# Kernel optimization log

Hardware: AMD Instinct MI355X
Metric: run time of the kernel (lower is better)

The kernel has to match this reference:

```python
import jax, jax.numpy as jnp
import numpy as np
import math

HEAD_DIM = 128
N_HEADS = 32
N_KV_HEADS = 8
HIDDEN = 4096
ROPE_BASE = 10000.0


def _rope_cos_sin(position_ids):
    # inv_freq: [D/2]
    inv_freq = 1.0 / (ROPE_BASE ** (jnp.arange(0, HEAD_DIM, 2, dtype=jnp.float32) / HEAD_DIM))
    freqs = position_ids.astype(jnp.float32)[..., None] * inv_freq  # [B,S,D/2]
    emb = jnp.concatenate([freqs, freqs], axis=-1)  # [B,S,D]
    return jnp.cos(emb), jnp.sin(emb)


def _rotate_half(x):
    x1, x2 = jnp.split(x, 2, axis=-1)
    return jnp.concatenate([-x2, x1], axis=-1)


def setup_inputs() -> dict:
    key = jax.random.key(0)
    ks = jax.random.split(key, 5)
    B, S = 1, 2048
    inp = {
        "hidden_states": jax.random.normal(ks[0], (B, S, HIDDEN), dtype=jnp.float32),
        "position_ids": jnp.arange(B * S, dtype=jnp.int32).reshape(B, S),
        "Wq": jax.random.normal(ks[1], (HIDDEN, N_HEADS * HEAD_DIM), dtype=jnp.float32) * 0.02,
        "Wk": jax.random.normal(ks[2], (HIDDEN, N_KV_HEADS * HEAD_DIM), dtype=jnp.float32) * 0.02,
        "Wv": jax.random.normal(ks[3], (HIDDEN, N_KV_HEADS * HEAD_DIM), dtype=jnp.float32) * 0.02,
        "Wo": jax.random.normal(ks[4], (N_HEADS * HEAD_DIM, HIDDEN), dtype=jnp.float32) * 0.02,
    }
    return inp


def reference(hidden_states, position_ids, Wq, Wk, Wv, Wo):
    B, S, _ = hidden_states.shape
    G = N_HEADS // N_KV_HEADS

    q = (hidden_states @ Wq).reshape(B, S, N_HEADS, HEAD_DIM).transpose(0, 2, 1, 3)      # [B,H,S,D]
    k = (hidden_states @ Wk).reshape(B, S, N_KV_HEADS, HEAD_DIM).transpose(0, 2, 1, 3)   # [B,Hkv,S,D]
    v = (hidden_states @ Wv).reshape(B, S, N_KV_HEADS, HEAD_DIM).transpose(0, 2, 1, 3)

    cos, sin = _rope_cos_sin(position_ids)          # [B,S,D]
    cos = cos[:, None, :, :]                         # [B,1,S,D]
    sin = sin[:, None, :, :]
    q = q * cos + _rotate_half(q) * sin
    k = k * cos + _rotate_half(k) * sin

    # GQA head expansion (repeat_interleave over head dim)
    k = jnp.repeat(k, G, axis=1)                     # [B,H,S,D]
    v = jnp.repeat(v, G, axis=1)

    scale = 1.0 / math.sqrt(HEAD_DIM)
    scores = jnp.einsum("bhqd,bhkd->bhqk", q, k) * scale  # [B,H,S,S]
    causal = jnp.triu(jnp.full((S, S), -jnp.inf, dtype=scores.dtype), k=1)
    scores = scores + causal[None, None]
    probs = jax.nn.softmax(scores.astype(jnp.float32), axis=-1).astype(q.dtype)
    ctx = jnp.einsum("bhqk,bhkd->bhqd", probs, v)    # [B,H,S,D]
    ctx = ctx.transpose(0, 2, 1, 3).reshape(B, S, N_HEADS * HEAD_DIM)
    return ctx @ Wo
```

## Files before the change

### kernel.cpp

```cpp
#include <hip/hip_runtime.h>
#include <hip/hip_bf16.h>
#include <math.h>

#define SEQ 2048
#define NHEADS 32
#define NKVH 8
#define HD 128
#define HIDDEN 4096

typedef unsigned short u16;
typedef unsigned int u32;
typedef __attribute__((ext_vector_type(8))) __bf16 bf16x8;
typedef __attribute__((ext_vector_type(4))) float f32x4;
typedef __attribute__((ext_vector_type(4))) u16 u16x4;
typedef __attribute__((ext_vector_type(4))) u32 u32x4;

__device__ __forceinline__ u16 f2bf(float f) {
  u32 u = __builtin_bit_cast(u32, f);
  u32 r = (u + 0x7fffu + ((u >> 16) & 1u)) >> 16;
  return (u16)r;
}
__device__ __forceinline__ float bf2f(u16 h) {
  return __builtin_bit_cast(float, ((u32)h) << 16);
}
__device__ __forceinline__ void gload_lds16(const void* g, void* l) {
  __builtin_amdgcn_global_load_lds(
      (const __attribute__((address_space(1))) u32*)g,
      (__attribute__((address_space(3))) u32*)l, 16, 0, 0);
}

__global__ void __launch_bounds__(256) conv_f2b_vec(const float* __restrict__ in,
                                                    u16* __restrict__ out, const int n) {
  const int i = (blockIdx.x * 256 + threadIdx.x) * 4;
  if (i >= n) return;
  const float4 v = *(const float4*)(in + i);
  u16x4 o;
  o.x = f2bf(v.x); o.y = f2bf(v.y); o.z = f2bf(v.z); o.w = f2bf(v.w);
  *(u16x4*)(out + i) = o;
}

__global__ void __launch_bounds__(256) trans_f2b(const float* __restrict__ in,
                                                 u16* __restrict__ out, const int R, const int C) {
  __shared__ float tile[32][33];
  const int c0 = blockIdx.x * 32, r0 = blockIdx.y * 32;
  const int tx = threadIdx.x & 31, ty = threadIdx.x >> 5;
#pragma unroll
  for (int i = 0; i < 4; ++i)
    tile[ty + i * 8][tx] = in[(size_t)(r0 + ty + i * 8) * C + c0 + tx];
  __syncthreads();
#pragma unroll
  for (int i = 0; i < 4; ++i)
    out[(size_t)(c0 + ty + i * 8) * R + r0 + tx] = f2bf(tile[tx][ty + i * 8]);
}

__global__ void __launch_bounds__(256) trans_b2b(const u16* __restrict__ in,
                                                 u16* __restrict__ out, const int R, const int C) {
  __shared__ u16 tile[32][34];
  const int c0 = blockIdx.x * 32, r0 = blockIdx.y * 32;
  const int tx = threadIdx.x & 31, ty = threadIdx.x >> 5;
#pragma unroll
  for (int i = 0; i < 4; ++i)
    tile[ty + i * 8][tx] = in[(size_t)(r0 + ty + i * 8) * C + c0 + tx];
  __syncthreads();
#pragma unroll
  for (int i = 0; i < 4; ++i)
    out[(size_t)(c0 + ty + i * 8) * R + r0 + tx] = tile[tx][ty + i * 8];
}

__global__ void __launch_bounds__(256) rope_ip(u16* __restrict__ x, const int* __restrict__ pos,
                                               const int lognh, const float oscale) {
  const int idx = blockIdx.x * 256 + threadIdx.x;
  const int j = idx & 63;
  const int hh = (idx >> 6) & ((1 << lognh) - 1);
  const int s = idx >> (6 + lognh);
  if (s >= SEQ) return;
  const float p = (float)pos[s];
  const float invf = __expf((float)j * -0.14391156831212787f);
  const float ang = p * invf;
  const float c = cosf(ang), sn = sinf(ang);
  u16* bp = x + ((size_t)s << (7 + lognh)) + hh * 128 + j;
  const float x1 = bf2f(bp[0]), x2 = bf2f(bp[64]);
  bp[0] = f2bf((x1 * c - x2 * sn) * oscale);
  bp[64] = f2bf((x2 * c + x1 * sn) * oscale);
}

template <int MF, int MH, int NH>
__device__ __forceinline__ void mfmaq(f32x4 (&acc)[MF][4], const bf16x8 (&af)[MF / 2][2],
                                      const bf16x8 (&bfv)[2][2]) {
#pragma unroll
  for (int f = 0; f < MF / 2; ++f)
#pragma unroll
    for (int e = 0; e < 2; ++e)
#pragma unroll
      for (int ks = 0; ks < 2; ++ks)
        acc[MH * (MF / 2) + f][NH * 2 + e] = __builtin_amdgcn_mfma_f32_16x16x32_bf16(
            af[f][ks], bfv[e][ks], acc[MH * (MF / 2) + f][NH * 2 + e], 0, 0, 0);
}

template <int MF>
__global__ void __launch_bounds__(512, 2) gemm8p(
    const u16* __restrict__ A, const u16* __restrict__ B0q, const u16* __restrict__ B1q,
    const u16* __restrict__ B2q, void* __restrict__ C0, void* __restrict__ C1,
    void* __restrict__ C2, const int K, const int n0t, const int n1t,
    const int N0, const int N1, const int N2, const int write_f32) {
  constexpr int BM = MF * 32;
  constexpr int AHR = BM / 2;
  constexpr int GA = (AHR * 128) / 8192;
  __shared__ u16 As[2][2][AHR * 64];
  __shared__ u16 Bs[2][2][128 * 64];

  const int t = threadIdx.x;
  const int lane = t & 63;
  const int w = t >> 6;
  const int wr = w >> 2;
  const int wc = w & 3;
  const int l15 = lane & 15, l4 = lane >> 4;

  const int nxt = gridDim.x;
  int flat = blockIdx.y * nxt + blockIdx.x;
  flat = (flat & 7) * ((nxt * (int)gridDim.y) >> 3) + (flat >> 3);
  int bxt = flat % nxt;
  const int byt = flat / nxt;

  const u16* Bp; char* Cw; int Nn;
  if (bxt < n0t) { Bp = B0q; Cw = (char*)C0; Nn = N0; }
  else if (bxt < n0t + n1t) { bxt -= n0t; Bp = B1q; Cw = (char*)C1; Nn = N1; }
  else { bxt -= n0t + n1t; Bp = B2q; Cw = (char*)C2; Nn = N2; }
  const int row0 = byt * BM, col0 = bxt * 256;

  auto stageA = [&](int buf, int half, int tile) {
#pragma unroll
    for (int g = 0; g < GA; ++g) {
      const int o = (g * 512 + t) * 16;
      const int ridx = o >> 7;
      const int slot = (o >> 4) & 7;
      const int gr = (ridx / (MF * 8)) * AHR + half * (MF * 8) + (ridx % (MF * 8));
      gload_lds16(A + (size_t)(row0 + gr) * K + (tile << 6) + ((slot ^ (ridx & 7)) << 3),
                  (char*)&As[buf][half][0] + o);
    }
  };
  auto stageB = [&](int buf, int half, int tile) {
#pragma unroll
    for (int g = 0; g < 2; ++g) {
      const int o = (g * 512 + t) * 16;
      const int ridx = o >> 7;
      const int slot = (o >> 4) & 7;
      const int gn = (ridx >> 5) * 64 + half * 32 + (ridx & 31);
      gload_lds16(Bp + (size_t)(col0 + gn) * K + (tile << 6) + ((slot ^ (ridx & 7)) << 3),
                  (char*)&Bs[buf][half][0] + o);
    }
  };

  bf16x8 af[MF / 2][2], bfv[2][2];
  auto loadA = [&](int buf, int half) {
#pragma unroll
    for (int f = 0; f < MF / 2; ++f)
#pragma unroll
      for (int ks = 0; ks < 2; ++ks) {
        const int idx = wr * (MF * 8) + f * 16 + l15;
        af[f][ks] = *(const bf16x8*)((const char*)&As[buf][half][0] + idx * 128 +
                                     (((ks * 4 + l4) ^ (idx & 7)) << 4));
      }
  };
  auto loadB = [&](int buf, int half) {
#pragma unroll
    for (int e = 0; e < 2; ++e)
#pragma unroll
      for (int ks = 0; ks < 2; ++ks) {
        const int idx = wc * 32 + e * 16 + l15;
        bfv[e][ks] = *(const bf16x8*)((const char*)&Bs[buf][half][0] + idx * 128 +
                                      (((ks * 4 + l4) ^ (idx & 7)) << 4));
      }
  };

  f32x4 acc[MF][4];
#pragma unroll
  for (int m_ = 0; m_ < MF; ++m_)
#pragma unroll
    for (int n_ = 0; n_ < 4; ++n_) acc[m_][n_] = f32x4{0.f, 0.f, 0.f, 0.f};

  const int nkt = K >> 6, nit = nkt >> 1;

#define VMW_STEADY                                                  \
  if constexpr (MF == 8) asm volatile("s_waitcnt vmcnt(4)" ::: "memory"); \
  else asm volatile("s_waitcnt vmcnt(3)" ::: "memory");
#define BAR __builtin_amdgcn_s_barrier()
#define PRIO1 __builtin_amdgcn_s_setprio(1)
#define PRIO0 __builtin_amdgcn_s_setprio(0)

  stageA(0, 0, 0); stageA(0, 1, 0); stageB(0, 0, 0); stageB(0, 1, 0);
  stageA(1, 0, 1); stageB(1, 1, 1);
  VMW_STEADY;
  BAR;

  for (int i = 0; i < nit; ++i) {
    const int tb = 2 * i;
    const bool g2 = (i + 1 < nit);
    loadA(0, 0); loadB(0, 0);
    stageA(1, 1, tb + 1);
    BAR; PRIO1; mfmaq<MF, 0, 0>(acc, af, bfv); PRIO0; BAR;
    loadB(0, 1);
    stageB(1, 0, tb + 1);
    BAR; PRIO1; mfmaq<MF, 0, 1>(acc, af, bfv); PRIO0; BAR;
    loadA(0, 1);
    if (g2) stageA(0, 0, tb + 2);
    BAR; PRIO1; mfmaq<MF, 1, 1>(acc, af, bfv); PRIO0; BAR;
    loadB(0, 0);
    if (g2) stageB(0, 1, tb + 2);
    BAR; PRIO1; mfmaq<MF, 1, 0>(acc, af, bfv); PRIO0;
    if (g2) { VMW_STEADY; } else { asm volatile("s_waitcnt vmcnt(0)" ::: "memory"); }
    BAR;
    loadA(1, 0); loadB(1, 0);
    if (g2) stageA(0, 1, tb + 2);
    BAR; PRIO1; mfmaq<MF, 0, 0>(acc, af, bfv); PRIO0; BAR;
    loadB(1, 1);
    if (g2) stageB(0, 0, tb + 2);
    BAR; PRIO1; mfmaq<MF, 0, 1>(acc, af, bfv); PRIO0; BAR;
    loadA(1, 1);
    if (g2) stageA(1, 0, tb + 3);
    BAR; PRIO1; mfmaq<MF, 1, 1>(acc, af, bfv); PRIO0; BAR;
    loadB(1, 0);
    if (g2) stageB(1, 1, tb + 3);
    BAR; PRIO1; mfmaq<MF, 1, 0>(acc, af, bfv); PRIO0;
    if (g2) { VMW_STEADY; } else { asm volatile("s_waitcnt vmcnt(0)" ::: "memory"); }
    BAR;
  }
#undef VMW_STEADY
#undef BAR
#undef PRIO1
#undef PRIO0

  if (write_f32) {
    float* C = (float*)Cw;
#pragma unroll
    for (int am = 0; am < MF; ++am) {
      const int row = row0 + wr * AHR + (am / (MF / 2)) * (MF * 8) + (am % (MF / 2)) * 16 + l4 * 4;
#pragma unroll
      for (int an = 0; an < 4; ++an) {
        const int col = col0 + wc * 64 + (an >> 1) * 32 + (an & 1) * 16 + l15;
#pragma unroll
        for (int r = 0; r < 4; ++r)
          C[(size_t)(row + r) * Nn + col] = acc[am][an][r];
      }
    }
  } else {
    u16* C = (u16*)Cw;
#pragma unroll
    for (int am = 0; am < MF; ++am) {
      const int row = row0 + wr * AHR + (am / (MF / 2)) * (MF * 8) + (am % (MF / 2)) * 16 + l4 * 4;
#pragma unroll
      for (int an = 0; an < 4; ++an) {
        const int col = col0 + wc * 64 + (an >> 1) * 32 + (an & 1) * 16 + l15;
#pragma unroll
        for (int r = 0; r < 4; ++r)
          C[(size_t)(row + r) * Nn + col] = f2bf(acc[am][an][r]);
      }
    }
  }
}

__device__ __forceinline__ void stage_kv(const u16* __restrict__ k, const u16* __restrict__ vt,
                                         const int kvh, const int kv0, u16* KsB, u16* VsB,
                                         const int t) {
#pragma unroll
  for (int i = 0; i < 4; ++i) {
    const int o = (i * 256 + t) * 16;
    const int row = o >> 8;
    const int slot = (o >> 4) & 15;
    gload_lds16(k + (size_t)(kv0 + row) * (NKVH * HD) + kvh * HD + ((slot ^ (row & 7)) << 3),
                (char*)KsB + o);
  }
#pragma unroll
  for (int i = 0; i < 4; ++i) {
    const int o = (i * 256 + t) * 16;
    const int row = o >> 7;
    const int slot = (o >> 4) & 7;
    gload_lds16(vt + (size_t)(kvh * HD + row) * SEQ + kv0 + ((slot ^ (row & 7)) << 3),
                (char*)VsB + o);
  }
}

__global__ void __launch_bounds__(256) attn_fwd(const u16* __restrict__ q, const u16* __restrict__ k,
                                                const u16* __restrict__ vt, u16* __restrict__ ctx) {
  __shared__ u16 Ks[2][64 * 128];
  __shared__ u16 Vs[2][128 * 64];
  const int t = threadIdx.x, lane = t & 63, w = t >> 6;
  const int h = blockIdx.x;
  const int qb = (int)gridDim.y - 1 - (int)blockIdx.y;
  const int kvh = h >> 2;
  const int q0 = qb * 64;
  const int sq_base = q0 + w * 16;
  const int l15 = lane & 15, l4 = lane >> 4;
  const int sq_abs = sq_base + l15;

  bf16x8 qf[4];
  {
    const u16* qp = q + (size_t)sq_abs * (NHEADS * HD) + h * HD + l4 * 8;
#pragma unroll
    for (int kb = 0; kb < 4; ++kb) qf[kb] = *(const bf16x8*)(qp + kb * 32);
  }
  f32x4 po[8];
#pragma unroll
  for (int i = 0; i < 8; ++i) po[i] = f32x4{0.f, 0.f, 0.f, 0.f};
  float mrow = -1e30f;
  float lrow = 0.f;

  const int nb = qb + 1;
  stage_kv(k, vt, kvh, 0, Ks[0], Vs[0], t);
  __syncthreads();
  int cur = 0;

  for (int b = 0; b < nb; ++b) {
    if (b + 1 < nb) stage_kv(k, vt, kvh, (b + 1) * 64, Ks[cur ^ 1], Vs[cur ^ 1], t);

    f32x4 st[4];
#pragma unroll
    for (int c = 0; c < 4; ++c) st[c] = f32x4{0.f, 0.f, 0.f, 0.f};
#pragma unroll
    for (int c = 0; c < 4; ++c) {
      const int row = c * 16 + l15;
#pragma unroll
      for (int kb = 0; kb < 4; ++kb) {
        const int slot = kb * 4 + l4;
        bf16x8 bk = *(const bf16x8*)((const char*)Ks[cur] + row * 256 + ((slot ^ (row & 7)) << 4));
        st[c] = __builtin_amdgcn_mfma_f32_16x16x32_bf16(bk, qf[kb], st[c], 0, 0, 0);
      }
    }

    if (b == nb - 1) {
#pragma unroll
      for (int c = 0; c < 4; ++c)
#pragma unroll
        for (int r = 0; r < 4; ++r) {
          const int sk = b * 64 + c * 16 + l4 * 4 + r;
          if (sk > sq_abs) st[c][r] = -1e30f;
        }
    }

    float rmax = -3e38f;
#pragma unroll
    for (int c = 0; c < 4; ++c)
      rmax = fmaxf(rmax, fmaxf(fmaxf(st[c][0], st[c][1]), fmaxf(st[c][2], st[c][3])));
    rmax = fmaxf(rmax, __shfl_xor(rmax, 16, 64));
    rmax = fmaxf(rmax, __shfl_xor(rmax, 32, 64));

    const bool skip = __all(rmax <= mrow + 8.f);
    const float mnew = skip ? mrow : fmaxf(mrow, rmax);

    float rs = 0.f;
#pragma unroll
    for (int c = 0; c < 4; ++c) {
      const float e0 = exp2f(st[c][0] - mnew), e1 = exp2f(st[c][1] - mnew);
      const float e2 = exp2f(st[c][2] - mnew), e3 = exp2f(st[c][3] - mnew);
      st[c][0] = e0; st[c][1] = e1; st[c][2] = e2; st[c][3] = e3;
      rs += (e0 + e1) + (e2 + e3);
    }
    rs += __shfl_xor(rs, 16, 64);
    rs += __shfl_xor(rs, 32, 64);

    if (!skip) {
      const float alpha = exp2f(mrow - mnew);
      mrow = mnew;
      lrow = lrow * alpha + rs;
      float av[4];
#pragma unroll
      for (int r = 0; r < 4; ++r) av[r] = __shfl(alpha, l4 * 4 + r, 16);
#pragma unroll
      for (int db = 0; db < 8; ++db)
#pragma unroll
        for (int r = 0; r < 4; ++r) po[db][r] *= av[r];
    } else {
      lrow += rs;
    }

    u32 pk[4][2];
#pragma unroll
    for (int c = 0; c < 4; ++c) {
      pk[c][0] = (u32)f2bf(st[c][0]) | ((u32)f2bf(st[c][1]) << 16);
      pk[c][1] = (u32)f2bf(st[c][2]) | ((u32)f2bf(st[c][3]) << 16);
    }
    const int src01 = l15 + ((lane & 16) << 1);
    const int src23 = src01 + 16;
    const bool lo = (lane & 32) == 0;
#pragma unroll
    for (int kb2 = 0; kb2 < 2; ++kb2) {
      const int c0 = kb2 * 2, c1 = c0 + 1;
      const u32 a0 = (u32)__shfl((int)pk[c0][0], src01, 64);
      const u32 a1 = (u32)__shfl((int)pk[c0][1], src01, 64);
      const u32 a2 = (u32)__shfl((int)pk[c0][0], src23, 64);
      const u32 a3 = (u32)__shfl((int)pk[c0][1], src23, 64);
      const u32 b0 = (u32)__shfl((int)pk[c1][0], src01, 64);
      const u32 b1 = (u32)__shfl((int)pk[c1][1], src01, 64);
      const u32 b2 = (u32)__shfl((int)pk[c1][0], src23, 64);
      const u32 b3 = (u32)__shfl((int)pk[c1][1], src23, 64);
      u32x4 wq;
      wq.x = lo ? a0 : b0;
      wq.y = lo ? a1 : b1;
      wq.z = lo ? a2 : b2;
      wq.w = lo ? a3 : b3;
      const bf16x8 pa = __builtin_bit_cast(bf16x8, wq);
#pragma unroll
      for (int db = 0; db < 8; ++db) {
        const int vrow = db * 16 + l15;
        const int pslot = kb2 * 4 + l4;
        bf16x8 bv = *(const bf16x8*)((const char*)Vs[cur] + vrow * 128 + ((pslot ^ (vrow & 7)) << 4));
        po[db] = __builtin_amdgcn_mfma_f32_16x16x32_bf16(pa, bv, po[db], 0, 0, 0);
      }
    }
    __syncthreads();
    cur ^= 1;
  }

  float rl[4];
#pragma unroll
  for (int r = 0; r < 4; ++r) rl[r] = 1.f / __shfl(lrow, l4 * 4 + r, 16);
#pragma unroll
  for (int db = 0; db < 8; ++db)
#pragma unroll
    for (int r = 0; r < 4; ++r) {
      const int sq = sq_base + l4 * 4 + r;
      const int d = db * 16 + l15;
      ctx[(size_t)sq * (NHEADS * HD) + h * HD + d] = f2bf(po[db][r] * rl[r]);
    }
}

extern "C" void kernel_launch(void* const* d_in, const int* in_sizes, int n_in,
                              void* d_out, int out_size, void* d_ws, size_t ws_size,
                              hipStream_t stream) {
  const float* hs = (const float*)d_in[0];
  const int* pos = (const int*)d_in[1];
  const float* Wq = (const float*)d_in[2];
  const float* Wk = (const float*)d_in[3];
  const float* Wv = (const float*)d_in[4];
  const float* Wo = (const float*)d_in[5];

  u16* ws = (u16*)d_ws;
  u16* Xb = ws;
  u16* Wqt = Xb + (size_t)2048 * 4096;
  u16* Wkt = Wqt + (size_t)4096 * 4096;
  u16* Wvt = Wkt + (size_t)1024 * 4096;
  u16* Wot = Wvt + (size_t)1024 * 4096;
  u16* qb = Wot + (size_t)4096 * 4096;
  u16* kb = qb + (size_t)2048 * 4096;
  u16* vb = kb + (size_t)2048 * 1024;
  u16* vtb = vb + (size_t)2048 * 1024;
  u16* ctx = vtb + (size_t)1024 * 2048;
  const size_t need = ((size_t)(ctx - ws) + (size_t)2048 * 4096) * 2;
  if (ws_size < need) return;

  conv_f2b_vec<<<8192, 256, 0, stream>>>(hs, Xb, 2048 * 4096);
  trans_f2b<<<dim3(128, 128), 256, 0, stream>>>(Wq, Wqt, 4096, 4096);
  trans_f2b<<<dim3(32, 128), 256, 0, stream>>>(Wk, Wkt, 4096, 1024);
  trans_f2b<<<dim3(32, 128), 256, 0, stream>>>(Wv, Wvt, 4096, 1024);
  trans_f2b<<<dim3(128, 128), 256, 0, stream>>>(Wo, Wot, 4096, 4096);

  gemm8p<8><<<dim3(24, 8), 512, 0, stream>>>(Xb, Wqt, Wkt, Wvt, qb, kb, vb,
                                             4096, 16, 4, 4096, 1024, 1024, 0);

  const float qscale = 0.08838834764831845f * 1.44269504088896340f;
  rope_ip<<<16384, 256, 0, stream>>>(qb, pos, 5, qscale);
  rope_ip<<<4096, 256, 0, stream>>>(kb, pos, 3, 1.0f);

  trans_b2b<<<dim3(32, 64), 256, 0, stream>>>(vb, vtb, 2048, 1024);

  attn_fwd<<<dim3(32, 32), 256, 0, stream>>>(qb, kb, vtb, ctx);

  gemm8p<4><<<dim3(16, 16), 512, 0, stream>>>(ctx, Wot, Wot, Wot, d_out, d_out, d_out,
                                              4096, 16, 0, 4096, 4096, 4096, 1);
}
```

Baseline: 375.7 us.

## Switch QKV GEMM to 32x32 MFMA and overlap Wo transpose in spare blocks

Rewrites the fused QKV projection GEMM to use 32x32x16 bf16 MFMA instructions with per-wave 128x64 tiles instead of 16x16x32. This reduces LDS fragment reads per flop and the MFMA issue count. The grid is padded from 192 to 256 blocks, and the 64 extra blocks do the Wo fp32-to-bf16 transpose, which removes a separate launch and fills otherwise idle CUs. The output GEMM becomes a specialized non-templated kernel. The transpose blocks run a serial 64-step loop and could become the tail of the QKV launch.

```diff
diff --git a/kernel.cpp b/kernel.cpp
--- a/kernel.cpp
+++ b/kernel.cpp
@@ -12,6 +12,7 @@
 typedef unsigned int u32;
 typedef __attribute__((ext_vector_type(8))) __bf16 bf16x8;
 typedef __attribute__((ext_vector_type(4))) float f32x4;
+typedef __attribute__((ext_vector_type(16))) float f32x16;
 typedef __attribute__((ext_vector_type(4))) u16 u16x4;
 typedef __attribute__((ext_vector_type(4))) u32 u32x4;
 
@@ -28,6 +29,11 @@
       (const __attribute__((address_space(1))) u32*)g,
       (__attribute__((address_space(3))) u32*)l, 16, 0, 0);
 }
+
+#define BAR __builtin_amdgcn_s_barrier()
+#define PRIO1 __builtin_amdgcn_s_setprio(1)
+#define PRIO0 __builtin_amdgcn_s_setprio(0)
+#define VMW(n) asm volatile("s_waitcnt vmcnt(" #n ")" ::: "memory")
 
 __global__ void __launch_bounds__(256) conv_f2b_vec(const float* __restrict__ in,
                                                     u16* __restrict__ out, const int n) {
@@ -84,58 +90,66 @@
   bp[64] = f2bf((x2 * c + x1 * sn) * oscale);
 }
 
-template <int MF, int MH, int NH>
-__device__ __forceinline__ void mfmaq(f32x4 (&acc)[MF][4], const bf16x8 (&af)[MF / 2][2],
-                                      const bf16x8 (&bfv)[2][2]) {
-#pragma unroll
-  for (int f = 0; f < MF / 2; ++f)
-#pragma unroll
-    for (int e = 0; e < 2; ++e)
-#pragma unroll
-      for (int ks = 0; ks < 2; ++ks)
-        acc[MH * (MF / 2) + f][NH * 2 + e] = __builtin_amdgcn_mfma_f32_16x16x32_bf16(
-            af[f][ks], bfv[e][ks], acc[MH * (MF / 2) + f][NH * 2 + e], 0, 0, 0);
-}
-
-template <int MF>
-__global__ void __launch_bounds__(512, 2) gemm8p(
+template <int MH, int NH>
+__device__ __forceinline__ void mfq32(f32x16 (&acc)[4][2], const bf16x8 (&afr)[2][4],
+                                      const bf16x8 (&b)[4]) {
+#pragma unroll
+  for (int f = 0; f < 2; ++f)
+#pragma unroll
+    for (int ks = 0; ks < 4; ++ks)
+      acc[MH * 2 + f][NH] = __builtin_amdgcn_mfma_f32_32x32x16_bf16(
+          afr[f][ks], b[ks], acc[MH * 2 + f][NH], 0, 0, 0);
+}
+
+__global__ void __launch_bounds__(512, 2) gemm8p32(
     const u16* __restrict__ A, const u16* __restrict__ B0q, const u16* __restrict__ B1q,
-    const u16* __restrict__ B2q, void* __restrict__ C0, void* __restrict__ C1,
-    void* __restrict__ C2, const int K, const int n0t, const int n1t,
-    const int N0, const int N1, const int N2, const int write_f32) {
-  constexpr int BM = MF * 32;
-  constexpr int AHR = BM / 2;
-  constexpr int GA = (AHR * 128) / 8192;
-  __shared__ u16 As[2][2][AHR * 64];
+    const u16* __restrict__ B2q, u16* __restrict__ C0, u16* __restrict__ C1,
+    u16* __restrict__ C2, const float* __restrict__ Wsrc, u16* __restrict__ Wdst) {
+  __shared__ u16 As[2][2][128 * 64];
   __shared__ u16 Bs[2][2][128 * 64];
-
   const int t = threadIdx.x;
-  const int lane = t & 63;
-  const int w = t >> 6;
-  const int wr = w >> 2;
-  const int wc = w & 3;
-  const int l15 = lane & 15, l4 = lane >> 4;
-
-  const int nxt = gridDim.x;
-  int flat = blockIdx.y * nxt + blockIdx.x;
-  flat = (flat & 7) * ((nxt * (int)gridDim.y) >> 3) + (flat >> 3);
-  int bxt = flat % nxt;
-  const int byt = flat / nxt;
-
-  const u16* Bp; char* Cw; int Nn;
-  if (bxt < n0t) { Bp = B0q; Cw = (char*)C0; Nn = N0; }
-  else if (bxt < n0t + n1t) { bxt -= n0t; Bp = B1q; Cw = (char*)C1; Nn = N1; }
-  else { bxt -= n0t + n1t; Bp = B2q; Cw = (char*)C2; Nn = N2; }
-  const int row0 = byt * BM, col0 = bxt * 256;
+  const int flat = blockIdx.x;
+  const int swz = (flat & 7) * 32 + (flat >> 3);
+
+  if (swz >= 192) {
+    const int wid = swz - 192;
+    float* tf = (float*)&As[0][0][0];
+    const int tx = t & 63, ty = t >> 6;
+    const int r0 = wid * 64;
+    for (int ct = 0; ct < 64; ++ct) {
+      const int c0 = ct * 64;
+#pragma unroll
+      for (int i = 0; i < 8; ++i)
+        tf[(ty + i * 8) * 65 + tx] = Wsrc[(size_t)(r0 + ty + i * 8) * 4096 + c0 + tx];
+      __syncthreads();
+#pragma unroll
+      for (int i = 0; i < 8; ++i)
+        Wdst[(size_t)(c0 + ty + i * 8) * 4096 + r0 + tx] = f2bf(tf[tx * 65 + ty + i * 8]);
+      __syncthreads();
+    }
+    return;
+  }
+
+  const int lane = t & 63, w = t >> 6;
+  const int wr = w >> 2, wc = w & 3;
+  const int l31 = lane & 31, l5 = lane >> 5;
+
+  int bxt = swz % 24;
+  const int byt = swz / 24;
+  const u16* Bp; u16* Cw; int Nn;
+  if (bxt < 16) { Bp = B0q; Cw = C0; Nn = 4096; }
+  else if (bxt < 20) { bxt -= 16; Bp = B1q; Cw = C1; Nn = 1024; }
+  else { bxt -= 20; Bp = B2q; Cw = C2; Nn = 1024; }
+  const int row0 = byt * 256, col0 = bxt * 256;
 
   auto stageA = [&](int buf, int half, int tile) {
 #pragma unroll
-    for (int g = 0; g < GA; ++g) {
+    for (int g = 0; g < 2; ++g) {
       const int o = (g * 512 + t) * 16;
       const int ridx = o >> 7;
       const int slot = (o >> 4) & 7;
-      const int gr = (ridx / (MF * 8)) * AHR + half * (MF * 8) + (ridx % (MF * 8));
-      gload_lds16(A + (size_t)(row0 + gr) * K + (tile << 6) + ((slot ^ (ridx & 7)) << 3),
+      const int gr = (ridx >> 6) * 128 + half * 64 + (ridx & 63);
+      gload_lds16(A + (size_t)(row0 + gr) * 4096 + (tile << 6) + ((slot ^ (ridx & 7)) << 3),
                   (char*)&As[buf][half][0] + o);
     }
   };
@@ -146,115 +160,218 @@
       const int ridx = o >> 7;
       const int slot = (o >> 4) & 7;
       const int gn = (ridx >> 5) * 64 + half * 32 + (ridx & 31);
-      gload_lds16(Bp + (size_t)(col0 + gn) * K + (tile << 6) + ((slot ^ (ridx & 7)) << 3),
+      gload_lds16(Bp + (size_t)(col0 + gn) * 4096 + (tile << 6) + ((slot ^ (ridx & 7)) << 3),
                   (char*)&Bs[buf][half][0] + o);
     }
   };
 
-  bf16x8 af[MF / 2][2], bfv[2][2];
-  auto loadA = [&](int buf, int half) {
-#pragma unroll
-    for (int f = 0; f < MF / 2; ++f)
-#pragma unroll
-      for (int ks = 0; ks < 2; ++ks) {
-        const int idx = wr * (MF * 8) + f * 16 + l15;
-        af[f][ks] = *(const bf16x8*)((const char*)&As[buf][half][0] + idx * 128 +
-                                     (((ks * 4 + l4) ^ (idx & 7)) << 4));
+  bf16x8 afr[2][4], bf0[4], bf1[4];
+  auto loadA32 = [&](int buf, int half) {
+#pragma unroll
+    for (int f = 0; f < 2; ++f)
+#pragma unroll
+      for (int ks = 0; ks < 4; ++ks) {
+        const int idx = wr * 64 + f * 32 + l31;
+        const int slot = ks * 2 + l5;
+        afr[f][ks] = *(const bf16x8*)((const char*)&As[buf][half][0] + idx * 128 +
+                                      ((slot ^ (idx & 7)) << 4));
       }
   };
-  auto loadB = [&](int buf, int half) {
-#pragma unroll
-    for (int e = 0; e < 2; ++e)
-#pragma unroll
-      for (int ks = 0; ks < 2; ++ks) {
-        const int idx = wc * 32 + e * 16 + l15;
-        bfv[e][ks] = *(const bf16x8*)((const char*)&Bs[buf][half][0] + idx * 128 +
-                                      (((ks * 4 + l4) ^ (idx & 7)) << 4));
-      }
-  };
-
-  f32x4 acc[MF][4];
-#pragma unroll
-  for (int m_ = 0; m_ < MF; ++m_)
-#pragma unroll
-    for (int n_ = 0; n_ < 4; ++n_) acc[m_][n_] = f32x4{0.f, 0.f, 0.f, 0.f};
-
-  const int nkt = K >> 6, nit = nkt >> 1;
-
-#define VMW_STEADY                                                  \
-  if constexpr (MF == 8) asm volatile("s_waitcnt vmcnt(4)" ::: "memory"); \
-  else asm volatile("s_waitcnt vmcnt(3)" ::: "memory");
-#define BAR __builtin_amdgcn_s_barrier()
-#define PRIO1 __builtin_amdgcn_s_setprio(1)
-#define PRIO0 __builtin_amdgcn_s_setprio(0)
+  auto loadB32 = [&](int buf, int half, bf16x8 (&dst)[4]) {
+#pragma unroll
+    for (int ks = 0; ks < 4; ++ks) {
+      const int idx = wc * 32 + l31;
+      const int slot = ks * 2 + l5;
+      dst[ks] = *(const bf16x8*)((const char*)&Bs[buf][half][0] + idx * 128 +
+                                 ((slot ^ (idx & 7)) << 4));
+    }
+  };
+
+  f32x16 acc[4][2];
+#pragma unroll
+  for (int m_ = 0; m_ < 4; ++m_)
+#pragma unroll
+    for (int n_ = 0; n_ < 2; ++n_)
+#pragma unroll
+      for (int e = 0; e < 16; ++e) acc[m_][n_][e] = 0.f;
+
+  const int nit = (4096 >> 6) >> 1;
 
   stageA(0, 0, 0); stageA(0, 1, 0); stageB(0, 0, 0); stageB(0, 1, 0);
   stageA(1, 0, 1); stageB(1, 1, 1);
-  VMW_STEADY;
+  VMW(4);
   BAR;
 
   for (int i = 0; i < nit; ++i) {
     const int tb = 2 * i;
     const bool g2 = (i + 1 < nit);
-    loadA(0, 0); loadB(0, 0);
+    loadA32(0, 0); loadB32(0, 0, bf0);
     stageA(1, 1, tb + 1);
-    BAR; PRIO1; mfmaq<MF, 0, 0>(acc, af, bfv); PRIO0; BAR;
-    loadB(0, 1);
+    BAR; PRIO1; mfq32<0, 0>(acc, afr, bf0); PRIO0; BAR;
+    loadB32(0, 1, bf1);
     stageB(1, 0, tb + 1);
-    BAR; PRIO1; mfmaq<MF, 0, 1>(acc, af, bfv); PRIO0; BAR;
+    BAR; PRIO1; mfq32<0, 1>(acc, afr, bf1); PRIO0; BAR;
+    loadA32(0, 1);
+    if (g2) stageA(0, 0, tb + 2);
+    BAR; PRIO1; mfq32<1, 1>(acc, afr, bf1); PRIO0; BAR;
+    if (g2) stageB(0, 1, tb + 2);
+    BAR; PRIO1; mfq32<1, 0>(acc, afr, bf0); PRIO0;
+    if (g2) { VMW(4); } else { VMW(0); }
+    BAR;
+    loadA32(1, 0); loadB32(1, 0, bf0);
+    if (g2) stageA(0, 1, tb + 2);
+    BAR; PRIO1; mfq32<0, 0>(acc, afr, bf0); PRIO0; BAR;
+    loadB32(1, 1, bf1);
+    if (g2) stageB(0, 0, tb + 2);
+    BAR; PRIO1; mfq32<0, 1>(acc, afr, bf1); PRIO0; BAR;
+    loadA32(1, 1);
+    if (g2) stageA(1, 0, tb + 3);
+    BAR; PRIO1; mfq32<1, 1>(acc, afr, bf1); PRIO0; BAR;
+    if (g2) stageB(1, 1, tb + 3);
+    BAR; PRIO1; mfq32<1, 0>(acc, afr, bf0); PRIO0;
+    if (g2) { VMW(4); } else { VMW(0); }
+    BAR;
+  }
+
+#pragma unroll
+  for (int am = 0; am < 4; ++am)
+#pragma unroll
+    for (int an = 0; an < 2; ++an) {
+      const int colb = col0 + wc * 64 + an * 32 + l31;
+#pragma unroll
+      for (int q = 0; q < 4; ++q) {
+        const int rowb = row0 + wr * 128 + am * 32 + q * 8 + l5 * 4;
+#pragma unroll
+        for (int rr = 0; rr < 4; ++rr)
+          Cw[(size_t)(rowb + rr) * Nn + colb] = f2bf(acc[am][an][q * 4 + rr]);
+      }
+    }
+}
+
+template <int MH, int NH>
+__device__ __forceinline__ void mfq16(f32x4 (&acc)[4][4], const bf16x8 (&af)[2][2],
+                                      const bf16x8 (&b)[2][2]) {
+#pragma unroll
+  for (int f = 0; f < 2; ++f)
+#pragma unroll
+    for (int e = 0; e < 2; ++e)
+#pragma unroll
+      for (int ks = 0; ks < 2; ++ks)
+        acc[MH * 2 + f][NH * 2 + e] = __builtin_amdgcn_mfma_f32_16x16x32_bf16(
+            af[f][ks], b[e][ks], acc[MH * 2 + f][NH * 2 + e], 0, 0, 0);
+}
+
+__global__ void __launch_bounds__(512, 2) gemm8p16(
+    const u16* __restrict__ A, const u16* __restrict__ B, float* __restrict__ C) {
+  __shared__ u16 As[2][2][64 * 64];
+  __shared__ u16 Bs[2][2][128 * 64];
+  const int t = threadIdx.x;
+  const int lane = t & 63, w = t >> 6;
+  const int wr = w >> 2, wc = w & 3;
+  const int l15 = lane & 15, l4 = lane >> 4;
+
+  const int flat = blockIdx.x;
+  const int swz = (flat & 7) * 32 + (flat >> 3);
+  const int bxt = swz & 15, byt = swz >> 4;
+  const int row0 = byt * 128, col0 = bxt * 256;
+
+  auto stageA = [&](int buf, int half, int tile) {
+    const int o = t * 16;
+    const int ridx = o >> 7;
+    const int slot = (o >> 4) & 7;
+    const int gr = (ridx >> 5) * 64 + half * 32 + (ridx & 31);
+    gload_lds16(A + (size_t)(row0 + gr) * 4096 + (tile << 6) + ((slot ^ (ridx & 7)) << 3),
+                (char*)&As[buf][half][0] + o);
+  };
+  auto stageB = [&](int buf, int half, int tile) {
+#pragma unroll
+    for (int g = 0; g < 2; ++g) {
+      const int o = (g * 512 + t) * 16;
+      const int ridx = o >> 7;
+      const int slot = (o >> 4) & 7;
+      const int gn = (ridx >> 5) * 64 + half * 32 + (ridx & 31);
+      gload_lds16(B + (size_t)(col0 + gn) * 4096 + (tile << 6) + ((slot ^ (ridx & 7)) << 3),
+                  (char*)&Bs[buf][half][0] + o);
+    }
+  };
+
+  bf16x8 af[2][2], bf0[2][2], bf1[2][2];
+  auto loadA = [&](int buf, int half) {
+#pragma unroll
+    for (int f = 0; f < 2; ++f)
+#pragma unroll
+      for (int ks = 0; ks < 2; ++ks) {
+        const int idx = wr * 32 + f * 16 + l15;
+        const int slot = ks * 4 + l4;
+        af[f][ks] = *(const bf16x8*)((const char*)&As[buf][half][0] + idx * 128 +
+                                     ((slot ^ (idx & 7)) << 4));
+      }
+  };
+  auto loadB = [&](int buf, int half, bf16x8 (&dst)[2][2]) {
+#pragma unroll
+    for (int e = 0; e < 2; ++e)
+#pragma unroll
+      for (int ks = 0; ks < 2; ++ks) {
+        const int idx = wc * 32 + e * 16 + l15;
+        const int slot = ks * 4 + l4;
+        dst[e][ks] = *(const bf16x8*)((const char*)&Bs[buf][half][0] + idx * 128 +
+                                      ((slot ^ (idx & 7)) << 4));
+      }
+  };
+
+  f32x4 acc[4][4];
+#pragma unroll
+  for (int m_ = 0; m_ < 4; ++m_)
+#pragma unroll
+    for (int n_ = 0; n_ < 4; ++n_) acc[m_][n_] = f32x4{0.f, 0.f, 0.f, 0.f};
+
+  const int nit = (4096 >> 6) >> 1;
+
+  stageA(0, 0, 0); stageA(0, 1, 0); stageB(0, 0, 0); stageB(0, 1, 0);
+  stageA(1, 0, 1); stageB(1, 1, 1);
+  VMW(3);
+  BAR;
+
+  for (int i = 0; i < nit; ++i) {
+    const int tb = 2 * i;
+    const bool g2 = (i + 1 < nit);
+    loadA(0, 0); loadB(0, 0, bf0);
+    stageA(1, 1, tb + 1);
+    BAR; PRIO1; mfq16<0, 0>(acc, af, bf0); PRIO0; BAR;
+    loadB(0, 1, bf1);
+    stageB(1, 0, tb + 1);
+    BAR; PRIO1; mfq16<0, 1>(acc, af, bf1); PRIO0; BAR;
     loadA(0, 1);
     if (g2) stageA(0, 0, tb + 2);
-    BAR; PRIO1; mfmaq<MF, 1, 1>(acc, af, bfv); PRIO0; BAR;
-    loadB(0, 0);
+    BAR; PRIO1; mfq16<1, 1>(acc, af, bf1); PRIO0; BAR;
     if (g2) stageB(0, 1, tb + 2);
-    BAR; PRIO1; mfmaq<MF, 1, 0>(acc, af, bfv); PRIO0;
-    if (g2) { VMW_STEADY; } else { asm volatile("s_waitcnt vmcnt(0)" ::: "memory"); }
+    BAR; PRIO1; mfq16<1, 0>(acc, af, bf0); PRIO0;
+    if (g2) { VMW(3); } else { VMW(0); }
     BAR;
-    loadA(1, 0); loadB(1, 0);
+    loadA(1, 0); loadB(1, 0, bf0);
     if (g2) stageA(0, 1, tb + 2);
-    BAR; PRIO1; mfmaq<MF, 0, 0>(acc, af, bfv); PRIO0; BAR;
-    loadB(1, 1);
+    BAR; PRIO1; mfq16<0, 0>(acc, af, bf0); PRIO0; BAR;
+    loadB(1, 1, bf1);
     if (g2) stageB(0, 0, tb + 2);
-    BAR; PRIO1; mfmaq<MF, 0, 1>(acc, af, bfv); PRIO0; BAR;
+    BAR; PRIO1; mfq16<0, 1>(acc, af, bf1); PRIO0; BAR;
     loadA(1, 1);
     if (g2) stageA(1, 0, tb + 3);
-    BAR; PRIO1; mfmaq<MF, 1, 1>(acc, af, bfv); PRIO0; BAR;
-    loadB(1, 0);
+    BAR; PRIO1; mfq16<1, 1>(acc, af, bf1); PRIO0; BAR;
     if (g2) stageB(1, 1, tb + 3);
-    BAR; PRIO1; mfmaq<MF, 1, 0>(acc, af, bfv); PRIO0;
-    if (g2) { VMW_STEADY; } else { asm volatile("s_waitcnt vmcnt(0)" ::: "memory"); }
+    BAR; PRIO1; mfq16<1, 0>(acc, af, bf0); PRIO0;
+    if (g2) { VMW(3); } else { VMW(0); }
     BAR;
   }
-#undef VMW_STEADY
-#undef BAR
-#undef PRIO1
-#undef PRIO0
-
-  if (write_f32) {
-    float* C = (float*)Cw;
-#pragma unroll
-    for (int am = 0; am < MF; ++am) {
-      const int row = row0 + wr * AHR + (am / (MF / 2)) * (MF * 8) + (am % (MF / 2)) * 16 + l4 * 4;
-#pragma unroll
-      for (int an = 0; an < 4; ++an) {
-        const int col = col0 + wc * 64 + (an >> 1) * 32 + (an & 1) * 16 + l15;
-#pragma unroll
-        for (int r = 0; r < 4; ++r)
-          C[(size_t)(row + r) * Nn + col] = acc[am][an][r];
-      }
-    }
-  } else {
-    u16* C = (u16*)Cw;
-#pragma unroll
-    for (int am = 0; am < MF; ++am) {
-      const int row = row0 + wr * AHR + (am / (MF / 2)) * (MF * 8) + (am % (MF / 2)) * 16 + l4 * 4;
-#pragma unroll
-      for (int an = 0; an < 4; ++an) {
-        const int col = col0 + wc * 64 + (an >> 1) * 32 + (an & 1) * 16 + l15;
-#pragma unroll
-        for (int r = 0; r < 4; ++r)
-          C[(size_t)(row + r) * Nn + col] = f2bf(acc[am][an][r]);
-      }
+
+#pragma unroll
+  for (int am = 0; am < 4; ++am) {
+    const int rowb = row0 + wr * 64 + (am >> 1) * 32 + (am & 1) * 16 + l4 * 4;
+#pragma unroll
+    for (int an = 0; an < 4; ++an) {
+      const int colb = col0 + wc * 64 + (an >> 1) * 32 + (an & 1) * 16 + l15;
+#pragma unroll
+      for (int r = 0; r < 4; ++r)
+        C[(size_t)(rowb + r) * 4096 + colb] = acc[am][an][r];
     }
   }
 }
@@ -452,10 +569,8 @@
   trans_f2b<<<dim3(128, 128), 256, 0, stream>>>(Wq, Wqt, 4096, 4096);
   trans_f2b<<<dim3(32, 128), 256, 0, stream>>>(Wk, Wkt, 4096, 1024);
   trans_f2b<<<dim3(32, 128), 256, 0, stream>>>(Wv, Wvt, 4096, 1024);
-  trans_f2b<<<dim3(128, 128), 256, 0, stream>>>(Wo, Wot, 4096, 4096);
-
-  gemm8p<8><<<dim3(24, 8), 512, 0, stream>>>(Xb, Wqt, Wkt, Wvt, qb, kb, vb,
-                                             4096, 16, 4, 4096, 1024, 1024, 0);
+
+  gemm8p32<<<256, 512, 0, stream>>>(Xb, Wqt, Wkt, Wvt, qb, kb, vb, Wo, Wot);
 
   const float qscale = 0.08838834764831845f * 1.44269504088896340f;
   rope_ip<<<16384, 256, 0, stream>>>(qb, pos, 5, qscale);
@@ -465,6 +580,5 @@
 
   attn_fwd<<<dim3(32, 32), 256, 0, stream>>>(qb, kb, vtb, ctx);
 
-  gemm8p<4><<<dim3(16, 16), 512, 0, stream>>>(ctx, Wot, Wot, Wot, d_out, d_out, d_out,
-                                              4096, 16, 0, 4096, 4096, 4096, 1);
-}
+  gemm8p16<<<256, 512, 0, stream>>>(ctx, Wot, (float*)d_out);
+}
```

Result: faster. 351.5 us (-6.4%).
